# Kernel tuning notes

Hardware: AMD Instinct MI355X
Metric: run time of the kernel (lower is better)

## Reference

```python
import jax, jax.numpy as jnp
import numpy as np

NQ = 4          # number of qubits (hardcoded in the original module)
LET = 'pqrs'    # einsum letters for the 4 qubit axes


def setup_inputs() -> dict:
    key = jax.random.key(0)
    k1, k2 = jax.random.split(key)
    B = 1048576  # 2^20 samples
    x = jax.random.normal(k1, (B, NQ), dtype=jnp.float32)          # RX angles per sample
    weights = jax.random.normal(k2, (3, NQ, 3), dtype=jnp.float32) * 0.1  # (layers, wires, 3)
    return {"x": x, "weights": weights}


def _apply_1q(state, U, w):
    # state: (B,2,2,2,2) complex, U: (2,2) complex, applied on wire w
    sub = 'b' + LET
    out = sub.replace(LET[w], 'x')
    return jnp.einsum(f'x{LET[w]},{sub}->{out}', U, state)


def _cnot(state, c, t):
    # CNOT control c -> target t: flip target axis on the control=1 half
    s0, s1 = jnp.split(state, 2, axis=1 + c)
    s1 = jnp.flip(s1, axis=1 + t)
    return jnp.concatenate([s0, s1], axis=1 + c)


def _rot(phi, theta, omega):
    # PennyLane Rot(phi, theta, omega) = RZ(omega) RY(theta) RZ(phi)
    c = jnp.cos(theta * 0.5)
    s = jnp.sin(theta * 0.5)
    m00 = jnp.exp(-0.5j * (phi + omega)) * c
    m01 = -jnp.exp(0.5j * (phi - omega)) * s
    m10 = jnp.exp(-0.5j * (phi - omega)) * s
    m11 = jnp.exp(0.5j * (phi + omega)) * c
    return jnp.stack([jnp.stack([m00, m01]), jnp.stack([m10, m11])]).astype(jnp.complex64)


def _forward(x, weights):
    # --- RX(x_i) on |0>^4: product state, built as an outer product ---
    c = jnp.cos(x * 0.5)
    s = jnp.sin(x * 0.5)
    mi = np.complex64(-1j)
    vs = [jnp.stack([c[:, i].astype(jnp.complex64), mi * s[:, i]], axis=-1) for i in range(NQ)]
    state = jnp.einsum('bp,bq,br,bs->bpqrs', *vs)  # (B,2,2,2,2) complex64

    # --- StronglyEntanglingLayers (default ranges r = l % (NQ-1) + 1) ---
    n_layers = weights.shape[0]
    for l in range(n_layers):
        for i in range(NQ):
            U = _rot(weights[l, i, 0], weights[l, i, 1], weights[l, i, 2])
            state = _apply_1q(state, U, i)
        r = (l % (NQ - 1)) + 1
        for i in range(NQ):
            state = _cnot(state, i, (i + r) % NQ)

    # --- <Z_i> expectation values ---
    probs = state.real ** 2 + state.imag ** 2  # (B,2,2,2,2) float32
    outs = []
    for w in range(NQ):
        axes = tuple(a for a in range(1, NQ + 1) if a != w + 1)
        m = probs.sum(axis=axes)  # (B,2) marginal over wire w
        outs.append(m[:, 0] - m[:, 1])
    return jnp.stack(outs, axis=-1)  # (B, NQ)


def reference(x, weights):
    return _forward(x, weights)
```

## Files before the change

### kernel.cpp

```cpp
#include <hip/hip_runtime.h>
#include <hip/hip_bf16.h>


__global__ void build_V_kernel(const float* __restrict__ w, float* __restrict__ V) {
    int k = threadIdx.x;
    if (k >= 16) return;

    float ar[16], ai[16];
#pragma unroll
    for (int j = 0; j < 16; ++j) { ar[j] = (j == k) ? 1.f : 0.f; ai[j] = 0.f; }

#pragma unroll
    for (int l = 0; l < 3; ++l) {
#pragma unroll
        for (int i = 0; i < 4; ++i) {
            float phi = w[l * 12 + i * 3 + 0];
            float th  = w[l * 12 + i * 3 + 1];
            float om  = w[l * 12 + i * 3 + 2];
            float ct = cosf(0.5f * th), st = sinf(0.5f * th);
            float alpha = 0.5f * (phi + om), beta = 0.5f * (phi - om);
            float sa, ca, sb, cb;
            sincosf(alpha, &sa, &ca);
            sincosf(beta,  &sb, &cb);
            float m00r =  ca * ct, m00i = -sa * ct;
            float m01r = -cb * st, m01i = -sb * st;
            float m10r =  cb * st, m10i = -sb * st;
            float m11r =  ca * ct, m11i =  sa * ct;
            int mask = 1 << i;
#pragma unroll
            for (int j = 0; j < 16; ++j) {
                if (j & mask) continue;
                int j1 = j | mask;
                float a0r = ar[j],  a0i = ai[j];
                float a1r = ar[j1], a1i = ai[j1];
                ar[j]  = m00r * a0r - m00i * a0i + m01r * a1r - m01i * a1i;
                ai[j]  = m00r * a0i + m00i * a0r + m01r * a1i + m01i * a1r;
                ar[j1] = m10r * a0r - m10i * a0i + m11r * a1r - m11i * a1i;
                ai[j1] = m10r * a0i + m10i * a0r + m11r * a1i + m11i * a1r;
            }
        }
        int r = (l % 3) + 1;
#pragma unroll
        for (int i = 0; i < 4; ++i) {
            int c = i, t = (i + r) & 3;
            int cm = 1 << c, tm = 1 << t;
#pragma unroll
            for (int j = 0; j < 16; ++j) {
                if ((j & cm) && !(j & tm)) {
                    int j2 = j | tm;
                    float tr = ar[j], ti = ai[j];
                    ar[j] = ar[j2]; ai[j] = ai[j2];
                    ar[j2] = tr;    ai[j2] = ti;
                }
            }
        }
    }

    int p = __popc(k) & 3;
    float pr = (p == 0) ? 1.f : (p == 2) ? -1.f : 0.f;
    float pi = (p == 1) ? -1.f : (p == 3) ? 1.f : 0.f;
#pragma unroll
    for (int j = 0; j < 16; ++j) {
        float vr = ar[j] * pr - ai[j] * pi;
        float vi = ar[j] * pi + ai[j] * pr;
        V[j * 32 + k]      = vr;
        V[j * 32 + 16 + k] = vi;
    }
}

#define SPT 4
#define BLOCK 256

template <bool GUARD>
__launch_bounds__(BLOCK)
__global__ void qlayer_kernel(const float* __restrict__ x,
                              const float* __restrict__ V,
                              float* __restrict__ out, int B) {
    const int base = blockIdx.x * (BLOCK * SPT) + threadIdx.x;

    float m[SPT][16];
    float z[SPT][4];

#pragma unroll
    for (int s = 0; s < SPT; ++s) {
        int idx = base + s * BLOCK;
        float4 xv;
        if (!GUARD || idx < B) xv = ((const float4*)x)[idx];
        else xv = make_float4(0.f, 0.f, 0.f, 0.f);
        float c0, s0, c1, s1, c2, s2, c3, s3;
        __sincosf(0.5f * xv.x, &s0, &c0);
        __sincosf(0.5f * xv.y, &s1, &c1);
        __sincosf(0.5f * xv.z, &s2, &c2);
        __sincosf(0.5f * xv.w, &s3, &c3);

        float* ms = m[s];
        ms[0] = c0; ms[1] = s0;
        ms[2] = ms[0] * s1; ms[3] = ms[1] * s1;
        ms[0] *= c1;        ms[1] *= c1;
#pragma unroll
        for (int k = 0; k < 4; ++k) { ms[4 + k] = ms[k] * s2; ms[k] *= c2; }
#pragma unroll
        for (int k = 0; k < 8; ++k) { ms[8 + k] = ms[k] * s3; ms[k] *= c3; }

        z[s][0] = z[s][1] = z[s][2] = z[s][3] = 0.f;
    }

#pragma unroll
    for (int j = 0; j < 16; ++j) {
        float re[SPT], im[SPT];
#pragma unroll
        for (int s = 0; s < SPT; ++s) { re[s] = 0.f; im[s] = 0.f; }
#pragma unroll
        for (int k = 0; k < 16; ++k) {
            const float vr = V[j * 32 + k];
            const float vi = V[j * 32 + 16 + k];
#pragma unroll
            for (int s = 0; s < SPT; ++s) {
                re[s] = fmaf(vr, m[s][k], re[s]);
                im[s] = fmaf(vi, m[s][k], im[s]);
            }
        }
#pragma unroll
        for (int s = 0; s < SPT; ++s) {
            float p = fmaf(re[s], re[s], im[s] * im[s]);
            z[s][0] += (j & 1) ? -p : p;
            z[s][1] += (j & 2) ? -p : p;
            z[s][2] += (j & 4) ? -p : p;
            z[s][3] += (j & 8) ? -p : p;
        }
    }

#pragma unroll
    for (int s = 0; s < SPT; ++s) {
        int idx = base + s * BLOCK;
        if (!GUARD || idx < B) {
            float4 o; o.x = z[s][0]; o.y = z[s][1]; o.z = z[s][2]; o.w = z[s][3];
            ((float4*)out)[idx] = o;
        }
    }
}

extern "C" void kernel_launch(void* const* d_in, const int* in_sizes, int n_in,
                              void* d_out, int out_size, void* d_ws, size_t ws_size,
                              hipStream_t stream) {
    const float* x = (const float*)d_in[0];
    const float* w = (const float*)d_in[1];
    float* out = (float*)d_out;
    float* V = (float*)d_ws;

    int B = in_sizes[0] / 4;

    build_V_kernel<<<1, 64, 0, stream>>>(w, V);

    const int spb = BLOCK * SPT;
    if (B % spb == 0) {
        qlayer_kernel<false><<<B / spb, BLOCK, 0, stream>>>(x, V, out, B);
    } else {
        qlayer_kernel<true><<<(B + spb - 1) / spb, BLOCK, 0, stream>>>(x, V, out, B);
    }
}
```

Measured before the change: 99.18 us.

## Precompute quadratic-form coefficients in trig basis to shrink per-sample math

The setup kernel now folds the circuit unitary and the Pauli-Z observables into 81 coefficient vectors, one per combination of {1, cos x, sin x} across the four input angles. The main kernel then evaluates each expectation as a short polynomial in the full-angle sines and cosines instead of building a 16-entry complex state and doing a 16x16 complex matrix-vector product per sample. The coefficients are staged in shared memory per block. This removes most per-sample FMAs in exchange for a larger setup kernel, a block-level barrier and some extra shared-memory traffic.

```diff
diff --git a/kernel.cpp b/kernel.cpp
--- a/kernel.cpp
+++ b/kernel.cpp
@@ -2,69 +2,114 @@
 #include <hip/hip_bf16.h>
 
 
-__global__ void build_V_kernel(const float* __restrict__ w, float* __restrict__ V) {
-    int k = threadIdx.x;
-    if (k >= 16) return;
-
-    float ar[16], ai[16];
-#pragma unroll
-    for (int j = 0; j < 16; ++j) { ar[j] = (j == k) ? 1.f : 0.f; ai[j] = 0.f; }
-
-#pragma unroll
-    for (int l = 0; l < 3; ++l) {
-#pragma unroll
-        for (int i = 0; i < 4; ++i) {
-            float phi = w[l * 12 + i * 3 + 0];
-            float th  = w[l * 12 + i * 3 + 1];
-            float om  = w[l * 12 + i * 3 + 2];
-            float ct = cosf(0.5f * th), st = sinf(0.5f * th);
-            float alpha = 0.5f * (phi + om), beta = 0.5f * (phi - om);
-            float sa, ca, sb, cb;
-            sincosf(alpha, &sa, &ca);
-            sincosf(beta,  &sb, &cb);
-            float m00r =  ca * ct, m00i = -sa * ct;
-            float m01r = -cb * st, m01i = -sb * st;
-            float m10r =  cb * st, m10i = -sb * st;
-            float m11r =  ca * ct, m11i =  sa * ct;
-            int mask = 1 << i;
-#pragma unroll
-            for (int j = 0; j < 16; ++j) {
-                if (j & mask) continue;
-                int j1 = j | mask;
-                float a0r = ar[j],  a0i = ai[j];
-                float a1r = ar[j1], a1i = ai[j1];
-                ar[j]  = m00r * a0r - m00i * a0i + m01r * a1r - m01i * a1i;
-                ai[j]  = m00r * a0i + m00i * a0r + m01r * a1i + m01i * a1r;
-                ar[j1] = m10r * a0r - m10i * a0i + m11r * a1r - m11i * a1i;
-                ai[j1] = m10r * a0i + m10i * a0r + m11r * a1i + m11i * a1r;
-            }
-        }
-        int r = (l % 3) + 1;
-#pragma unroll
-        for (int i = 0; i < 4; ++i) {
-            int c = i, t = (i + r) & 3;
-            int cm = 1 << c, tm = 1 << t;
-#pragma unroll
-            for (int j = 0; j < 16; ++j) {
-                if ((j & cm) && !(j & tm)) {
-                    int j2 = j | tm;
-                    float tr = ar[j], ti = ai[j];
-                    ar[j] = ar[j2]; ai[j] = ai[j2];
-                    ar[j2] = tr;    ai[j2] = ti;
+__global__ void build_C_kernel(const float* __restrict__ w, float4* __restrict__ C) {
+    __shared__ float Vr[16][16];
+    __shared__ float Vi[16][16];
+    __shared__ float A[4][16][16];
+
+    const int tid = threadIdx.x;
+
+    if (tid < 16) {
+        const int k = tid;
+        float ar[16], ai[16];
+#pragma unroll
+        for (int j = 0; j < 16; ++j) { ar[j] = (j == k) ? 1.f : 0.f; ai[j] = 0.f; }
+
+#pragma unroll
+        for (int l = 0; l < 3; ++l) {
+#pragma unroll
+            for (int i = 0; i < 4; ++i) {
+                float phi = w[l * 12 + i * 3 + 0];
+                float th  = w[l * 12 + i * 3 + 1];
+                float om  = w[l * 12 + i * 3 + 2];
+                float ct = cosf(0.5f * th), st = sinf(0.5f * th);
+                float alpha = 0.5f * (phi + om), beta = 0.5f * (phi - om);
+                float sa, ca, sb, cb;
+                sincosf(alpha, &sa, &ca);
+                sincosf(beta,  &sb, &cb);
+                float m00r =  ca * ct, m00i = -sa * ct;
+                float m01r = -cb * st, m01i = -sb * st;
+                float m10r =  cb * st, m10i = -sb * st;
+                float m11r =  ca * ct, m11i =  sa * ct;
+                int mask = 1 << i;
+#pragma unroll
+                for (int j = 0; j < 16; ++j) {
+                    if (j & mask) continue;
+                    int j1 = j | mask;
+                    float a0r = ar[j],  a0i = ai[j];
+                    float a1r = ar[j1], a1i = ai[j1];
+                    ar[j]  = m00r * a0r - m00i * a0i + m01r * a1r - m01i * a1i;
+                    ai[j]  = m00r * a0i + m00i * a0r + m01r * a1i + m01i * a1r;
+                    ar[j1] = m10r * a0r - m10i * a0i + m11r * a1r - m11i * a1i;
+                    ai[j1] = m10r * a0i + m10i * a0r + m11r * a1i + m11i * a1r;
                 }
             }
-        }
-    }
-
-    int p = __popc(k) & 3;
-    float pr = (p == 0) ? 1.f : (p == 2) ? -1.f : 0.f;
-    float pi = (p == 1) ? -1.f : (p == 3) ? 1.f : 0.f;
-#pragma unroll
-    for (int j = 0; j < 16; ++j) {
-        float vr = ar[j] * pr - ai[j] * pi;
-        float vi = ar[j] * pi + ai[j] * pr;
-        V[j * 32 + k]      = vr;
-        V[j * 32 + 16 + k] = vi;
+            int r = (l % 3) + 1;
+#pragma unroll
+            for (int i = 0; i < 4; ++i) {
+                int c = i, t = (i + r) & 3;
+                int cm = 1 << c, tm = 1 << t;
+#pragma unroll
+                for (int j = 0; j < 16; ++j) {
+                    if ((j & cm) && !(j & tm)) {
+                        int j2 = j | tm;
+                        float tr = ar[j], ti = ai[j];
+                        ar[j] = ar[j2]; ai[j] = ai[j2];
+                        ar[j2] = tr;    ai[j2] = ti;
+                    }
+                }
+            }
+        }
+
+        int p = __popc(k) & 3;
+        float pr = (p == 0) ? 1.f : (p == 2) ? -1.f : 0.f;
+        float pi = (p == 1) ? -1.f : (p == 3) ? 1.f : 0.f;
+#pragma unroll
+        for (int j = 0; j < 16; ++j) {
+            Vr[j][k] = ar[j] * pr - ai[j] * pi;
+            Vi[j][k] = ar[j] * pi + ai[j] * pr;
+        }
+    }
+    __syncthreads();
+
+    {
+        const int k = tid >> 4, l = tid & 15;
+        float acc0 = 0.f, acc1 = 0.f, acc2 = 0.f, acc3 = 0.f;
+#pragma unroll
+        for (int j = 0; j < 16; ++j) {
+            float p = Vr[j][k] * Vr[j][l] + Vi[j][k] * Vi[j][l];
+            acc0 += (j & 1) ? -p : p;
+            acc1 += (j & 2) ? -p : p;
+            acc2 += (j & 4) ? -p : p;
+            acc3 += (j & 8) ? -p : p;
+        }
+        A[0][k][l] = acc0; A[1][k][l] = acc1; A[2][k][l] = acc2; A[3][k][l] = acc3;
+    }
+    __syncthreads();
+
+    if (tid < 81) {
+        int d[4];
+        d[0] = tid % 3; d[1] = (tid / 3) % 3; d[2] = (tid / 9) % 3; d[3] = tid / 27;
+        float acc0 = 0.f, acc1 = 0.f, acc2 = 0.f, acc3 = 0.f;
+#pragma unroll
+        for (int o = 0; o < 16; ++o) {
+            int k = 0, l = 0; float sign = 1.f;
+#pragma unroll
+            for (int q = 0; q < 4; ++q) {
+                int oq = (o >> q) & 1;
+                if (d[q] == 2) { k |= oq << q; l |= (1 - oq) << q; }
+                else {
+                    k |= oq << q; l |= oq << q;
+                    if (d[q] == 1 && oq == 1) sign = -sign;
+                }
+            }
+            acc0 += sign * A[0][k][l];
+            acc1 += sign * A[1][k][l];
+            acc2 += sign * A[2][k][l];
+            acc3 += sign * A[3][k][l];
+        }
+        const float inv16 = 0.0625f;
+        C[tid] = make_float4(acc0 * inv16, acc1 * inv16, acc2 * inv16, acc3 * inv16);
     }
 }
 
@@ -74,11 +119,16 @@
 template <bool GUARD>
 __launch_bounds__(BLOCK)
 __global__ void qlayer_kernel(const float* __restrict__ x,
-                              const float* __restrict__ V,
+                              const float4* __restrict__ Cg,
                               float* __restrict__ out, int B) {
+    __shared__ float4 C[81];
+    if (threadIdx.x < 81) C[threadIdx.x] = Cg[threadIdx.x];
+    __syncthreads();
+
     const int base = blockIdx.x * (BLOCK * SPT) + threadIdx.x;
 
-    float m[SPT][16];
+    float c0[SPT], s0[SPT], c3[SPT], s3[SPT];
+    float G9[SPT][9];
     float z[SPT][4];
 
 #pragma unroll
@@ -87,46 +137,42 @@
         float4 xv;
         if (!GUARD || idx < B) xv = ((const float4*)x)[idx];
         else xv = make_float4(0.f, 0.f, 0.f, 0.f);
-        float c0, s0, c1, s1, c2, s2, c3, s3;
-        __sincosf(0.5f * xv.x, &s0, &c0);
-        __sincosf(0.5f * xv.y, &s1, &c1);
-        __sincosf(0.5f * xv.z, &s2, &c2);
-        __sincosf(0.5f * xv.w, &s3, &c3);
-
-        float* ms = m[s];
-        ms[0] = c0; ms[1] = s0;
-        ms[2] = ms[0] * s1; ms[3] = ms[1] * s1;
-        ms[0] *= c1;        ms[1] *= c1;
-#pragma unroll
-        for (int k = 0; k < 4; ++k) { ms[4 + k] = ms[k] * s2; ms[k] *= c2; }
-#pragma unroll
-        for (int k = 0; k < 8; ++k) { ms[8 + k] = ms[k] * s3; ms[k] *= c3; }
+
+        float c1, s1, c2, s2;
+        __sincosf(xv.x, &s0[s], &c0[s]);
+        __sincosf(xv.y, &s1, &c1);
+        __sincosf(xv.z, &s2, &c2);
+        __sincosf(xv.w, &s3[s], &c3[s]);
+
+        G9[s][0] = 1.f;     G9[s][1] = c1;      G9[s][2] = s1;
+        G9[s][3] = c2;      G9[s][4] = c1 * c2; G9[s][5] = s1 * c2;
+        G9[s][6] = s2;      G9[s][7] = c1 * s2; G9[s][8] = s1 * s2;
 
         z[s][0] = z[s][1] = z[s][2] = z[s][3] = 0.f;
     }
 
 #pragma unroll
-    for (int j = 0; j < 16; ++j) {
-        float re[SPT], im[SPT];
-#pragma unroll
-        for (int s = 0; s < SPT; ++s) { re[s] = 0.f; im[s] = 0.f; }
-#pragma unroll
-        for (int k = 0; k < 16; ++k) {
-            const float vr = V[j * 32 + k];
-            const float vi = V[j * 32 + 16 + k];
+    for (int t3 = 0; t3 < 3; ++t3) {
+#pragma unroll
+        for (int i9 = 0; i9 < 9; ++i9) {
+            const int combo = i9 + 9 * t3;
+            const float4 Ca = C[combo * 3 + 0];
+            const float4 Cb = C[combo * 3 + 1];
+            const float4 Cc = C[combo * 3 + 2];
 #pragma unroll
             for (int s = 0; s < SPT; ++s) {
-                re[s] = fmaf(vr, m[s][k], re[s]);
-                im[s] = fmaf(vi, m[s][k], im[s]);
-            }
-        }
-#pragma unroll
-        for (int s = 0; s < SPT; ++s) {
-            float p = fmaf(re[s], re[s], im[s] * im[s]);
-            z[s][0] += (j & 1) ? -p : p;
-            z[s][1] += (j & 2) ? -p : p;
-            z[s][2] += (j & 4) ? -p : p;
-            z[s][3] += (j & 8) ? -p : p;
+                float g = G9[s][i9];
+                if (t3 == 1) g *= c3[s];
+                if (t3 == 2) g *= s3[s];
+                float r0 = fmaf(c0[s], Cb.x, fmaf(s0[s], Cc.x, Ca.x));
+                float r1 = fmaf(c0[s], Cb.y, fmaf(s0[s], Cc.y, Ca.y));
+                float r2 = fmaf(c0[s], Cb.z, fmaf(s0[s], Cc.z, Ca.z));
+                float r3 = fmaf(c0[s], Cb.w, fmaf(s0[s], Cc.w, Ca.w));
+                z[s][0] = fmaf(g, r0, z[s][0]);
+                z[s][1] = fmaf(g, r1, z[s][1]);
+                z[s][2] = fmaf(g, r2, z[s][2]);
+                z[s][3] = fmaf(g, r3, z[s][3]);
+            }
         }
     }
 
@@ -146,16 +192,16 @@
     const float* x = (const float*)d_in[0];
     const float* w = (const float*)d_in[1];
     float* out = (float*)d_out;
-    float* V = (float*)d_ws;
+    float4* C = (float4*)d_ws;
 
     int B = in_sizes[0] / 4;
 
-    build_V_kernel<<<1, 64, 0, stream>>>(w, V);
+    build_C_kernel<<<1, 256, 0, stream>>>(w, C);
 
     const int spb = BLOCK * SPT;
     if (B % spb == 0) {
-        qlayer_kernel<false><<<B / spb, BLOCK, 0, stream>>>(x, V, out, B);
+        qlayer_kernel<false><<<B / spb, BLOCK, 0, stream>>>(x, C, out, B);
     } else {
-        qlayer_kernel<true><<<(B + spb - 1) / spb, BLOCK, 0, stream>>>(x, V, out, B);
+        qlayer_kernel<true><<<(B + spb - 1) / spb, BLOCK, 0, stream>>>(x, C, out, B);
     }
 }
```

After: 92.17 us. -7.1%, faster.
